# Performance work log

Hardware: AMD Instinct MI355X
Metric: run time of the kernel (lower is better)

Reference implementation:

```python
import jax, jax.numpy as jnp
from jax import lax
import numpy as np

B, L, NQ, NL, NC = 2048, 2048, 8, 3, 3  # batch, signal length, qubits, q-layers, classes


def setup_inputs() -> dict:
    key = jax.random.key(0)
    ks = jax.random.split(key, 20)
    rn = lambda k, shape, s=1.0: jax.random.normal(k, shape, jnp.float32) * s
    return dict(
        x_ecg=rn(ks[0], (B, 1, L)), x_eda=rn(ks[1], (B, 1, L)),
        x_emg=rn(ks[2], (B, 1, L)), x_resp=rn(ks[3], (B, 1, L)),
        conv1_w=rn(ks[4], (4, 16, 1, 3), 0.3), conv1_b=rn(ks[5], (4, 16), 0.05),
        conv2_w=rn(ks[6], (4, 32, 16, 3), 0.1), conv2_b=rn(ks[7], (4, 32), 0.05),
        lstm_w_ih=rn(ks[8], (4, 128, 32), 0.1), lstm_w_hh=rn(ks[9], (4, 128, 32), 0.1),
        lstm_b_ih=rn(ks[10], (4, 128), 0.05), lstm_b_hh=rn(ks[11], (4, 128), 0.05),
        bott_w=rn(ks[12], (8, 128), 0.08), bott_b=rn(ks[13], (8,), 0.05),
        q_weights=rn(ks[14], (NL, NQ, 3)),
        clf_w=rn(ks[15], (NC, 8), 0.3), clf_b=rn(ks[16], (NC,), 0.05),
    )


def _branch(x, c1w, c1b, c2w, c2b, wih, whh, bih, bhh):
    # x: [B,1,L]  ->  h_n: [B,32]
    dn = ('NCH', 'OIH', 'NCH')
    h = lax.conv_general_dilated(x, c1w, (1,), [(1, 1)], dimension_numbers=dn) + c1b[None, :, None]
    h = jax.nn.relu(h)
    h = h.reshape(h.shape[0], h.shape[1], -1, 2).max(-1)  # maxpool k=2
    h = lax.conv_general_dilated(h, c2w, (1,), [(1, 1)], dimension_numbers=dn) + c2b[None, :, None]
    h = jax.nn.relu(h)
    h = h.reshape(h.shape[0], h.shape[1], -1, 2).max(-1)  # [B,32,L//4]
    seq = jnp.swapaxes(h, 1, 2)  # [B,T,32]
    Bn, H = seq.shape[0], whh.shape[1]

    def step(carry, xt):
        hprev, cprev = carry
        gates = xt @ wih.T + hprev @ whh.T + bih + bhh  # [B,4H], torch gate order i,f,g,o
        i, f, g, o = jnp.split(gates, 4, axis=-1)
        c = jax.nn.sigmoid(f) * cprev + jax.nn.sigmoid(i) * jnp.tanh(g)
        hn = jax.nn.sigmoid(o) * jnp.tanh(c)
        return (hn, c), None

    init = (jnp.zeros((Bn, H), seq.dtype), jnp.zeros((Bn, H), seq.dtype))
    (h_n, _), _ = lax.scan(step, init, jnp.swapaxes(seq, 0, 1))
    return h_n


def _apply_1q(psi, gate, q, n):
    # psi: [B, 2^n]; gate: [2,2] (shared) or [B,2,2] (per-sample)
    Bn = psi.shape[0]
    left, right = 2 ** q, 2 ** (n - q - 1)
    s = psi.reshape(Bn, left, 2, right)
    if gate.ndim == 2:
        s = jnp.einsum('ij,bljr->blir', gate, s)
    else:
        s = jnp.einsum('bij,bljr->blir', gate, s)
    return s.reshape(Bn, -1)


def _apply_cnot(psi, c, t, n):
    # c < t always here
    Bn = psi.shape[0]
    s = psi.reshape(Bn, 2 ** c, 2, 2 ** (t - c - 1), 2, 2 ** (n - t - 1))
    s = s.at[:, :, 1].set(jnp.flip(s[:, :, 1], axis=3))
    return s.reshape(Bn, -1)


def _rz(a):
    e = jnp.exp(-0.5j * a)
    z = jnp.zeros_like(e)
    return jnp.stack([jnp.stack([e, z]), jnp.stack([z, jnp.conj(e)])])


def _ry(a):
    c, s = jnp.cos(a / 2), jnp.sin(a / 2)
    return jnp.stack([jnp.stack([c, -s]), jnp.stack([s, c])]).astype(jnp.complex64)


def _quantum(compressed, q_weights):
    # batched 8-qubit statevector simulation; compressed: [B, NQ]
    n = NQ
    Bn = compressed.shape[0]
    angles = compressed * jnp.pi
    psi = jnp.zeros((Bn, 2 ** n), jnp.complex64).at[:, 0].set(1.0)
    c, s = jnp.cos(angles / 2), jnp.sin(angles / 2)
    for q in range(n):  # RX embedding, per-sample gates
        g = jnp.stack([jnp.stack([c[:, q], -1j * s[:, q]], -1),
                       jnp.stack([-1j * s[:, q], c[:, q]], -1)], -2)  # [B,2,2]
        psi = _apply_1q(psi, g, q, n)
    for l in range(q_weights.shape[0]):
        for q in range(n):
            w = q_weights[l, q]
            # pennylane Rot(phi,theta,omega) = RZ(omega) @ RY(theta) @ RZ(phi)
            g = _rz(w[2]) @ _ry(w[1]) @ _rz(w[0])
            psi = _apply_1q(psi, g, q, n)
        stride = l + 1
        for q in range(n):
            t = q + stride
            if t < n:
                psi = _apply_cnot(psi, q, t, n)
    p = (jnp.abs(psi) ** 2).reshape((Bn,) + (2,) * n)
    zs = []
    for i in range(n):  # <Z_i> = P(|0>_i) - P(|1>_i)
        axes = tuple(a for a in range(1, n + 1) if a != i + 1)
        m = p.sum(axes)
        zs.append(m[:, 0] - m[:, 1])
    return jnp.stack(zs, -1).astype(jnp.float32)


def reference(x_ecg, x_eda, x_emg, x_resp, conv1_w, conv1_b, conv2_w, conv2_b,
              lstm_w_ih, lstm_w_hh, lstm_b_ih, lstm_b_hh, bott_w, bott_b,
              q_weights, clf_w, clf_b):
    xs = jnp.stack([x_ecg, x_eda, x_emg, x_resp])  # [4,B,1,L]
    feats = jax.vmap(_branch)(xs, conv1_w, conv1_b, conv2_w, conv2_b,
                              lstm_w_ih, lstm_w_hh, lstm_b_ih, lstm_b_hh)  # [4,B,32]
    combined = jnp.transpose(feats, (1, 0, 2)).reshape(feats.shape[1], -1)  # [B,128]
    compressed = jnp.tanh(combined @ bott_w.T + bott_b)  # [B,8]
    q_out = _quantum(compressed, q_weights)  # [B,8]
    logits = q_out @ clf_w.T + clf_b  # [B,3]
    return logits
```

## Files before the change

kernel.cpp:

```cpp
#include <hip/hip_runtime.h>
#include <hip/hip_bf16.h>

#define BATCH 2048
#define LSIG 2048
#define TSTEPS 512
#define CH 16
#define NCHUNK (TSTEPS / CH)

typedef float v2f __attribute__((ext_vector_type(2)));
typedef float v4f __attribute__((ext_vector_type(4)));
typedef __bf16 b16x8 __attribute__((ext_vector_type(8)));
typedef float f32x4 __attribute__((ext_vector_type(4)));
typedef unsigned int u32x4 __attribute__((ext_vector_type(4)));

#define PKFMA(d, a, b) asm("v_pk_fma_f32 %0, %1, %2, %0" : "+v"(d) : "v"(a), "v"(b))

__device__ __forceinline__ float sigf(float x) {
    return __fdividef(1.f, 1.f + __expf(-x));
}
__device__ __forceinline__ float tanhfast(float x) {
    return 1.f - __fdividef(2.f, __expf(2.f * x) + 1.f);
}
__device__ __forceinline__ unsigned short bf16rne(float f) {
    unsigned u = __float_as_uint(f);
    return (unsigned short)((u + 0x7FFFu + ((u >> 16) & 1u)) >> 16);
}
__device__ __forceinline__ unsigned cvtpk_bf16(float a, float b) {
    unsigned d;
    asm("v_cvt_pk_bf16_f32 %0, %1, %2" : "=v"(d) : "v"(a), "v"(b));
    return d;
}
__device__ __forceinline__ int swz(int co) {
    return (co < 16) ? ((co >> 2) * 8 + (co & 3))
                     : (((co >> 2) - 4) * 8 + 4 + (co & 3));
}

__global__ __launch_bounds__(64) void frontend_kernel(
    const float* __restrict__ x0, const float* __restrict__ x1,
    const float* __restrict__ x2, const float* __restrict__ x3,
    const float* __restrict__ c1w, const float* __restrict__ c1b,
    const float* __restrict__ c2w, const float* __restrict__ c2b,
    unsigned short* __restrict__ seqh, unsigned short* __restrict__ seql,
    int t0, int Tseg, int nck)
{
    const int s    = blockIdx.x;
    const int br   = blockIdx.y & 3;
    const int cko  = blockIdx.y >> 2;
    const int lane = threadIdx.x;
    const float* xg = (br == 0) ? x0 : (br == 1) ? x1 : (br == 2) ? x2 : x3;

    __shared__ float xs_c[70];
    __shared__ float p1buf[34][16];

    const int ci = lane & 15;
    const int co = lane & 31;
    const int hf = lane >> 5;
    const int sp = swz(co);

    const float w10 = c1w[br * 48 + ci * 3 + 0];
    const float w11 = c1w[br * 48 + ci * 3 + 1];
    const float w12 = c1w[br * 48 + ci * 3 + 2];
    const float b1v = c1b[br * 16 + ci];

    float wt[24];
    {
        const v4f* p = (const v4f*)(c2w + br * 1536 + co * 48 + hf * 24);
        #pragma unroll
        for (int i = 0; i < 6; ++i) ((v4f*)wt)[i] = p[i];
    }
    v4f w2p[3][2];
    #pragma unroll
    for (int k = 0; k < 3; ++k)
        #pragma unroll
        for (int h2 = 0; h2 < 2; ++h2)
            w2p[k][h2] = (v4f){ wt[(h2 * 4 + 0) * 3 + k], wt[(h2 * 4 + 1) * 3 + k],
                                wt[(h2 * 4 + 2) * 3 + k], wt[(h2 * 4 + 3) * 3 + k] };
    const float b2v = c2b[br * 32 + co];

    #pragma unroll 1
    for (int ic = 0; ic < nck; ++ic) {
        const int ck  = cko * nck + ic;
        const int tc0 = t0 + ck * CH;
        const int lt0 = ck * CH;

        __syncthreads();
        {
            int g = 4 * tc0 - 3 + lane;
            xs_c[lane] = ((unsigned)g < (unsigned)LSIG) ? xg[(size_t)s * LSIG + g] : 0.f;
            if (lane < 6) {
                int g2 = 4 * tc0 + 61 + lane;
                xs_c[64 + lane] = ((unsigned)g2 < (unsigned)LSIG) ? xg[(size_t)s * LSIG + g2] : 0.f;
            }
        }
        __syncthreads();

        #pragma unroll 1
        for (int it = 0; it < 9; ++it) {
            int idx = it * 64 + lane;
            if (idx < 34 * 16) {
                int pl = idx >> 4;
                float xa = xs_c[2 * pl + 0], xb = xs_c[2 * pl + 1];
                float xc = xs_c[2 * pl + 2], xd = xs_c[2 * pl + 3];
                float a0 = fmaf(xc, w12, fmaf(xb, w11, fmaf(xa, w10, b1v)));
                float a1 = fmaf(xd, w12, fmaf(xc, w11, fmaf(xb, w10, b1v)));
                float v = fmaxf(fmaxf(a0, a1), 0.f);
                int p1g = 2 * tc0 - 1 + pl;
                v = ((unsigned)p1g < (unsigned)(LSIG / 2)) ? v : 0.f;
                p1buf[pl][idx & 15] = v;
            }
        }
        __syncthreads();

        {
            const v4f* pbase = (const v4f*)&p1buf[0][0];
            const int h2o = hf * 2;
            v4f r0a = pbase[0 * 4 + h2o], r0b = pbase[0 * 4 + h2o + 1];
            v4f r1a = pbase[1 * 4 + h2o], r1b = pbase[1 * 4 + h2o + 1];
            v4f r2a = pbase[2 * 4 + h2o], r2b = pbase[2 * 4 + h2o + 1];
            v4f r3a = pbase[3 * 4 + h2o], r3b = pbase[3 * 4 + h2o + 1];
            #pragma unroll 1
            for (int tl = 0; tl < CH; ++tl) {
                v2f aA = {0.f, 0.f}, aB = {0.f, 0.f};
                PKFMA(aA, r0a.xy, w2p[0][0].xy); PKFMA(aA, r0a.zw, w2p[0][0].zw);
                PKFMA(aA, r0b.xy, w2p[0][1].xy); PKFMA(aA, r0b.zw, w2p[0][1].zw);
                PKFMA(aA, r1a.xy, w2p[1][0].xy); PKFMA(aA, r1a.zw, w2p[1][0].zw);
                PKFMA(aA, r1b.xy, w2p[1][1].xy); PKFMA(aA, r1b.zw, w2p[1][1].zw);
                PKFMA(aA, r2a.xy, w2p[2][0].xy); PKFMA(aA, r2a.zw, w2p[2][0].zw);
                PKFMA(aA, r2b.xy, w2p[2][1].xy); PKFMA(aA, r2b.zw, w2p[2][1].zw);
                PKFMA(aB, r1a.xy, w2p[0][0].xy); PKFMA(aB, r1a.zw, w2p[0][0].zw);
                PKFMA(aB, r1b.xy, w2p[0][1].xy); PKFMA(aB, r1b.zw, w2p[0][1].zw);
                PKFMA(aB, r2a.xy, w2p[1][0].xy); PKFMA(aB, r2a.zw, w2p[1][0].zw);
                PKFMA(aB, r2b.xy, w2p[1][1].xy); PKFMA(aB, r2b.zw, w2p[1][1].zw);
                PKFMA(aB, r3a.xy, w2p[2][0].xy); PKFMA(aB, r3a.zw, w2p[2][0].zw);
                PKFMA(aB, r3b.xy, w2p[2][1].xy); PKFMA(aB, r3b.zw, w2p[2][1].zw);
                float sA = aA.x + aA.y, sB = aB.x + aB.y;
                sA += __shfl_xor(sA, 32);
                sB += __shfl_xor(sB, 32);
                float sv = fmaxf(fmaxf(sA, sB) + b2v, 0.f);
                unsigned short hb = bf16rne(sv);
                float hif = __uint_as_float(((unsigned)hb) << 16);
                unsigned short lb = bf16rne(sv - hif);
                size_t off = (((size_t)br * Tseg + (lt0 + tl)) * 2048 + s) * 32 + sp;
                if (hf == 0) seqh[off] = hb;
                else         seql[off] = lb;
                r0a = r2a; r0b = r2b; r1a = r3a; r1b = r3b;
                if (tl < CH - 1) {
                    r2a = pbase[(2 * tl + 4) * 4 + h2o]; r2b = pbase[(2 * tl + 4) * 4 + h2o + 1];
                    r3a = pbase[(2 * tl + 5) * 4 + h2o]; r3b = pbase[(2 * tl + 5) * 4 + h2o + 1];
                }
            }
        }
    }
}

__global__ __launch_bounds__(64, 1) void lstm_mfma_kernel(
    const unsigned short* __restrict__ seqh, const unsigned short* __restrict__ seql,
    const float* __restrict__ wih, const float* __restrict__ whh,
    const float* __restrict__ bih, const float* __restrict__ bhh,
    float* __restrict__ state, float* __restrict__ feats,
    int t0, int Tseg)
{
    const int s0   = blockIdx.x * 16;
    const int br   = blockIdx.y;
    const int lane = threadIdx.x;
    const int c    = lane & 15;
    const int q    = lane >> 4;

    __shared__ f32x4 bias_lds[8][64];
    #pragma unroll
    for (int n = 0; n < 8; ++n) {
        f32x4 b;
        #pragma unroll
        for (int r = 0; r < 4; ++r) {
            int g = 16 * n + 4 * q + r;
            b[r] = bih[br * 128 + g] + bhh[br * 128 + g];
        }
        bias_lds[n][lane] = b;
    }
    __syncthreads();

    b16x8 wihhi[8], wihlo[8], whhhi[8], whhlo[8];
    #pragma unroll
    for (int n = 0; n < 8; ++n) {
        const int gr = 16 * n + c;
        const float* pi = wih + (size_t)br * 4096 + (size_t)gr * 32;
        const float* phw = whh + (size_t)br * 4096 + (size_t)gr * 32;
        v4f ia = *(const v4f*)(pi + 4 * q);
        v4f ib = *(const v4f*)(pi + 16 + 4 * q);
        v4f ha = *(const v4f*)(phw + 4 * q);
        v4f hb = *(const v4f*)(phw + 16 + 4 * q);
        #pragma unroll
        for (int j = 0; j < 4; ++j) {
            __bf16 t;
            t = (__bf16)ia[j]; wihhi[n][j]     = t; wihlo[n][j]     = (__bf16)(ia[j] - (float)t);
            t = (__bf16)ib[j]; wihhi[n][4 + j] = t; wihlo[n][4 + j] = (__bf16)(ib[j] - (float)t);
            t = (__bf16)ha[j]; whhhi[n][j]     = t; whhlo[n][j]     = (__bf16)(ha[j] - (float)t);
            t = (__bf16)hb[j]; whhhi[n][4 + j] = t; whhlo[n][4 + j] = (__bf16)(hb[j] - (float)t);
        }
    }

    b16x8 bhh_f, bhl_f;
    float cst[2][4];
    if (t0 == 0) {
        #pragma unroll
        for (int j = 0; j < 8; ++j) { bhh_f[j] = (__bf16)0.f; bhl_f[j] = (__bf16)0.f; }
        #pragma unroll
        for (int hh = 0; hh < 2; ++hh)
            #pragma unroll
            for (int r = 0; r < 4; ++r) cst[hh][r] = 0.f;
    } else {
        const float* st = state + (((size_t)br * BATCH + s0 + c) * 2) * 32;
        #pragma unroll
        for (int hh = 0; hh < 2; ++hh)
            #pragma unroll
            for (int r = 0; r < 4; ++r) {
                int u = 16 * hh + 4 * q + r;
                float hv = st[u];
                __bf16 hb2 = (__bf16)hv;
                bhh_f[hh * 4 + r] = hb2;
                bhl_f[hh * 4 + r] = (__bf16)(hv - (float)hb2);
                cst[hh][r] = st[32 + u];
            }
    }

    const size_t xbase = ((size_t)br * Tseg * 2048 + s0 + c) * 32 + (size_t)q * 8;
    const size_t xstep = 2048 * 32;
    const unsigned short* ph = seqh + xbase;
    const unsigned short* pl = seql + xbase;

    f32x4 xacc[8];
    b16x8 nh1, nl1;
    {
        b16x8 x0h = *(const b16x8*)ph;
        b16x8 x0l = *(const b16x8*)pl;
        #pragma unroll
        for (int n = 0; n < 8; ++n) {
            xacc[n] = __builtin_amdgcn_mfma_f32_16x16x32_bf16(wihhi[n], x0h, bias_lds[n][lane], 0, 0, 0);
            xacc[n] = __builtin_amdgcn_mfma_f32_16x16x32_bf16(wihhi[n], x0l, xacc[n], 0, 0, 0);
            xacc[n] = __builtin_amdgcn_mfma_f32_16x16x32_bf16(wihlo[n], x0h, xacc[n], 0, 0, 0);
        }
        nh1 = *(const b16x8*)(ph + xstep);
        nl1 = *(const b16x8*)(pl + xstep);
    }

#define STEP_BODY(LAST)                                                          \
    {                                                                            \
        _Pragma("unroll")                                                        \
        for (int n = 0; n < 8; ++n) {                                            \
            xacc[n] = __builtin_amdgcn_mfma_f32_16x16x32_bf16(whhhi[n], bhh_f, xacc[n], 0, 0, 0); \
            xacc[n] = __builtin_amdgcn_mfma_f32_16x16x32_bf16(whhhi[n], bhl_f, xacc[n], 0, 0, 0); \
            xacc[n] = __builtin_amdgcn_mfma_f32_16x16x32_bf16(whhlo[n], bhh_f, xacc[n], 0, 0, 0); \
        }                                                                        \
        float hv[8];                                                             \
        _Pragma("unroll")                                                        \
        for (int hh = 0; hh < 2; ++hh) {                                         \
            _Pragma("unroll")                                                    \
            for (int r = 0; r < 4; ++r) {                                        \
                float gi = xacc[0 + hh][r];                                      \
                float gf = xacc[2 + hh][r];                                      \
                float gg = xacc[4 + hh][r];                                      \
                float go = xacc[6 + hh][r];                                      \
                float si = sigf(gi);                                             \
                float sf = sigf(gf);                                             \
                float tg = tanhfast(gg);                                         \
                float so = sigf(go);                                             \
                float cc = fmaf(sf, cst[hh][r], si * tg);                        \
                cst[hh][r] = cc;                                                 \
                hv[hh * 4 + r] = so * tanhfast(cc);                              \
            }                                                                    \
        }                                                                        \
        u32x4 hd_, ld_;                                                          \
        _Pragma("unroll")                                                        \
        for (int p = 0; p < 4; ++p) {                                            \
            float a = hv[2 * p], b = hv[2 * p + 1];                              \
            unsigned d = cvtpk_bf16(a, b);                                       \
            float fa = __uint_as_float(d << 16);                                 \
            float fb = __uint_as_float(d & 0xFFFF0000u);                         \
            ld_[p] = cvtpk_bf16(a - fa, b - fb);                                 \
            hd_[p] = d;                                                          \
        }                                                                        \
        bhh_f = __builtin_bit_cast(b16x8, hd_);                                  \
        bhl_f = __builtin_bit_cast(b16x8, ld_);                                  \
        if (LAST) {                                                              \
            float* fp = feats + ((size_t)br * BATCH + s0 + c) * 32 + 4 * q;      \
            _Pragma("unroll")                                                    \
            for (int r = 0; r < 4; ++r) { fp[r] = hv[r]; fp[16 + r] = hv[4 + r]; } \
        }                                                                        \
    }

#define XACC_FROM(XH, XL)                                                        \
    {                                                                            \
        _Pragma("unroll")                                                        \
        for (int n = 0; n < 8; ++n) {                                            \
            xacc[n] = __builtin_amdgcn_mfma_f32_16x16x32_bf16(wihhi[n], XH, bias_lds[n][lane], 0, 0, 0); \
            xacc[n] = __builtin_amdgcn_mfma_f32_16x16x32_bf16(wihhi[n], XL, xacc[n], 0, 0, 0); \
            xacc[n] = __builtin_amdgcn_mfma_f32_16x16x32_bf16(wihlo[n], XH, xacc[n], 0, 0, 0); \
        }                                                                        \
    }

    #pragma unroll 1
    for (int t = 0; t < Tseg; t += 2) {
        b16x8 pbh, pbl;
        if (t + 2 < Tseg) {
            pbh = *(const b16x8*)(ph + (size_t)(t + 2) * xstep);
            pbl = *(const b16x8*)(pl + (size_t)(t + 2) * xstep);
        }
        STEP_BODY(false)
        XACC_FROM(nh1, nl1)

        const bool last = (t0 + t + 1 == TSTEPS - 1);
        if (t + 3 < Tseg) {
            nh1 = *(const b16x8*)(ph + (size_t)(t + 3) * xstep);
            nl1 = *(const b16x8*)(pl + (size_t)(t + 3) * xstep);
        }
        STEP_BODY(last)
        if (t + 2 < Tseg) { XACC_FROM(pbh, pbl) }
    }
#undef STEP_BODY
#undef XACC_FROM

    if (t0 + Tseg < TSTEPS) {
        float* st = state + (((size_t)br * BATCH + s0 + c) * 2) * 32;
        #pragma unroll
        for (int hh = 0; hh < 2; ++hh)
            #pragma unroll
            for (int r = 0; r < 4; ++r) {
                int u = 16 * hh + 4 * q + r;
                st[u]      = (float)bhh_f[hh * 4 + r] + (float)bhl_f[hh * 4 + r];
                st[32 + u] = cst[hh][r];
            }
    }
}

__global__ __launch_bounds__(64, 2) void branch_fallback(
    const float* __restrict__ x0, const float* __restrict__ x1,
    const float* __restrict__ x2, const float* __restrict__ x3,
    const float* __restrict__ c1w, const float* __restrict__ c1b,
    const float* __restrict__ c2w, const float* __restrict__ c2b,
    const float* __restrict__ wih, const float* __restrict__ whh,
    const float* __restrict__ bih, const float* __restrict__ bhh,
    float* __restrict__ feats)
{
    const int s    = blockIdx.x;
    const int br   = blockIdx.y;
    const int lane = threadIdx.x;
    const float* xg = (br == 0) ? x0 : (br == 1) ? x1 : (br == 2) ? x2 : x3;

    __shared__ float xs_c[70];
    __shared__ float p1buf[34][16];
    __shared__ float seqb[CH][32];
    __shared__ float hb[2][32];

    const int ci = lane & 15;
    const int co = lane & 31;
    const int hf = lane >> 5;

    const float bs0 = bih[br * 128 + lane]      + bhh[br * 128 + lane];
    const float bs1 = bih[br * 128 + lane + 64] + bhh[br * 128 + lane + 64];

    if (lane < 32) hb[0][lane] = 0.f;
    float c_state = 0.f;

    #pragma unroll 1
    for (int chk = 0; chk < NCHUNK; ++chk) {
        const int tc0 = chk * CH;
        {
            int g = 4 * tc0 - 3 + lane;
            xs_c[lane] = ((unsigned)g < (unsigned)LSIG) ? xg[(size_t)s * LSIG + g] : 0.f;
            if (lane < 6) {
                int g2 = 4 * tc0 + 61 + lane;
                xs_c[64 + lane] = ((unsigned)g2 < (unsigned)LSIG) ? xg[(size_t)s * LSIG + g2] : 0.f;
            }
        }
        const float* pc1 = c1w + br * 48 + ci * 3;  asm volatile("" : "+v"(pc1));
        const float w10 = pc1[0], w11 = pc1[1], w12 = pc1[2];
        const float* pb1 = c1b + br * 16 + ci;      asm volatile("" : "+v"(pb1));
        const float b1v = pb1[0];
        const float* pc2 = c2w + br * 1536 + co * 48 + hf * 24;
        asm volatile("" : "+v"(pc2));
        float wt[24];
        #pragma unroll
        for (int i = 0; i < 6; ++i) ((v4f*)wt)[i] = ((const v4f*)pc2)[i];
        v4f w2p[3][2];
        #pragma unroll
        for (int k = 0; k < 3; ++k)
            #pragma unroll
            for (int h2 = 0; h2 < 2; ++h2)
                w2p[k][h2] = (v4f){ wt[(h2 * 4 + 0) * 3 + k], wt[(h2 * 4 + 1) * 3 + k],
                                    wt[(h2 * 4 + 2) * 3 + k], wt[(h2 * 4 + 3) * 3 + k] };
        const float* pb2 = c2b + br * 32 + co;      asm volatile("" : "+v"(pb2));
        const float b2v = pb2[0];
        __syncthreads();
        #pragma unroll 1
        for (int it = 0; it < 9; ++it) {
            int idx = it * 64 + lane;
            if (idx < 34 * 16) {
                int pl = idx >> 4;
                float xa = xs_c[2 * pl + 0], xb = xs_c[2 * pl + 1];
                float xc = xs_c[2 * pl + 2], xd = xs_c[2 * pl + 3];
                float a0 = fmaf(xc, w12, fmaf(xb, w11, fmaf(xa, w10, b1v)));
                float a1 = fmaf(xd, w12, fmaf(xc, w11, fmaf(xb, w10, b1v)));
                float v = fmaxf(fmaxf(a0, a1), 0.f);
                int p1g = 2 * tc0 - 1 + pl;
                v = ((unsigned)p1g < (unsigned)(LSIG / 2)) ? v : 0.f;
                p1buf[pl][idx & 15] = v;
            }
        }
        __syncthreads();
        {
            const v4f* pbase = (const v4f*)&p1buf[0][0];
            const int h2o = hf * 2;
            v4f r0a = pbase[0 * 4 + h2o], r0b = pbase[0 * 4 + h2o + 1];
            v4f r1a = pbase[1 * 4 + h2o], r1b = pbase[1 * 4 + h2o + 1];
            v4f r2a = pbase[2 * 4 + h2o], r2b = pbase[2 * 4 + h2o + 1];
            v4f r3a = pbase[3 * 4 + h2o], r3b = pbase[3 * 4 + h2o + 1];
            #pragma unroll 1
            for (int tl = 0; tl < CH; ++tl) {
                v2f aA = {0.f, 0.f}, aB = {0.f, 0.f};
                PKFMA(aA, r0a.xy, w2p[0][0].xy); PKFMA(aA, r0a.zw, w2p[0][0].zw);
                PKFMA(aA, r0b.xy, w2p[0][1].xy); PKFMA(aA, r0b.zw, w2p[0][1].zw);
                PKFMA(aA, r1a.xy, w2p[1][0].xy); PKFMA(aA, r1a.zw, w2p[1][0].zw);
                PKFMA(aA, r1b.xy, w2p[1][1].xy); PKFMA(aA, r1b.zw, w2p[1][1].zw);
                PKFMA(aA, r2a.xy, w2p[2][0].xy); PKFMA(aA, r2a.zw, w2p[2][0].zw);
                PKFMA(aA, r2b.xy, w2p[2][1].xy); PKFMA(aA, r2b.zw, w2p[2][1].zw);
                PKFMA(aB, r1a.xy, w2p[0][0].xy); PKFMA(aB, r1a.zw, w2p[0][0].zw);
                PKFMA(aB, r1b.xy, w2p[0][1].xy); PKFMA(aB, r1b.zw, w2p[0][1].zw);
                PKFMA(aB, r2a.xy, w2p[1][0].xy); PKFMA(aB, r2a.zw, w2p[1][0].zw);
                PKFMA(aB, r2b.xy, w2p[1][1].xy); PKFMA(aB, r2b.zw, w2p[1][1].zw);
                PKFMA(aB, r3a.xy, w2p[2][0].xy); PKFMA(aB, r3a.zw, w2p[2][0].zw);
                PKFMA(aB, r3b.xy, w2p[2][1].xy); PKFMA(aB, r3b.zw, w2p[2][1].zw);
                float sA = aA.x + aA.y, sB = aB.x + aB.y;
                sA += __shfl_xor(sA, 32);
                sB += __shfl_xor(sB, 32);
                if (hf == 0)
                    seqb[tl][co] = fmaxf(fmaxf(sA, sB) + b2v, 0.f);
                r0a = r2a; r0b = r2b; r1a = r3a; r1b = r3b;
                if (tl < CH - 1) {
                    r2a = pbase[(2 * tl + 4) * 4 + h2o]; r2b = pbase[(2 * tl + 4) * 4 + h2o + 1];
                    r3a = pbase[(2 * tl + 5) * 4 + h2o]; r3b = pbase[(2 * tl + 5) * 4 + h2o + 1];
                }
            }
        }
        __syncthreads();
        float gpx0[CH], gpx1[CH];
        {
            const float* pwi = wih + (size_t)br * 4096 + (size_t)lane * 32;
            asm volatile("" : "+v"(pwi));
            v4f wiA[8], wiB[8];
            #pragma unroll
            for (int j = 0; j < 8; ++j) {
                wiA[j] = ((const v4f*)pwi)[j];
                wiB[j] = ((const v4f*)(pwi + 64 * 32))[j];
            }
            #pragma unroll
            for (int tl = 0; tl < CH; ++tl) {
                const v4f* xq = (const v4f*)&seqb[tl][0];
                v2f aA = {0.f, 0.f}, aB = {0.f, 0.f};
                #pragma unroll
                for (int j = 0; j < 8; ++j) {
                    v4f xv = xq[j];
                    PKFMA(aA, xv.xy, wiA[j].xy); PKFMA(aA, xv.zw, wiA[j].zw);
                    PKFMA(aB, xv.xy, wiB[j].xy); PKFMA(aB, xv.zw, wiB[j].zw);
                }
                gpx0[tl] = aA.x + aA.y;
                gpx1[tl] = aB.x + aB.y;
            }
        }
        {
            const float* pwh = whh + (size_t)br * 4096 + (size_t)lane * 32;
            asm volatile("" : "+v"(pwh));
            v4f whA[8], whB[8];
            #pragma unroll
            for (int j = 0; j < 8; ++j) {
                whA[j] = ((const v4f*)pwh)[j];
                whB[j] = ((const v4f*)(pwh + 64 * 32))[j];
            }
            #pragma unroll
            for (int tl = 0; tl < CH; ++tl) {
                __syncthreads();
                const int p = (tc0 + tl) & 1;
                const v4f* hq = (const v4f*)&hb[p][0];
                v2f aA = {0.f, 0.f}, aB = {0.f, 0.f};
                #pragma unroll
                for (int j = 0; j < 8; ++j) {
                    v4f hv = hq[j];
                    PKFMA(aA, hv.xy, whA[j].xy); PKFMA(aA, hv.zw, whA[j].zw);
                    PKFMA(aB, hv.xy, whB[j].xy); PKFMA(aB, hv.zw, whB[j].zw);
                }
                float g0 = bs0 + gpx0[tl] + aA.x + aA.y;
                float g1 = bs1 + gpx1[tl] + aB.x + aB.y;
                float a0 = sigf(g0);
                float earg = (lane < 32) ? 2.f * g1 : -g1;
                float e1 = __expf(fminf(earg, 80.f));
                float num = (lane < 32) ? e1 - 1.f : 1.f;
                float a1 = __fdividef(num, e1 + 1.f);
                float fa = __shfl_xor(a0, 32);
                float oa = __shfl_xor(a1, 32);
                if (lane < 32) {
                    c_state = fmaf(fa, c_state, a0 * a1);
                    hb[p ^ 1][lane] = oa * tanhfast(c_state);
                }
            }
        }
    }
    __syncthreads();
    if (lane < 32)
        feats[((size_t)br * BATCH + s) * 32 + lane] = hb[0][lane];
}


__device__ __forceinline__ void apply1q(float2* psi, int lane, int q,
                                        float2 g00, float2 g01,
                                        float2 g10, float2 g11)
{
    const int shift = 7 - q;
    const int right = 1 << shift;
    #pragma unroll
    for (int pp = 0; pp < 2; ++pp) {
        int p  = lane + 64 * pp;
        int l  = p >> shift;
        int r  = p & (right - 1);
        int i0 = (l << (shift + 1)) + r;
        int i1 = i0 + right;
        float2 a = psi[i0], b = psi[i1];
        float2 n0 = make_float2(g00.x * a.x - g00.y * a.y + g01.x * b.x - g01.y * b.y,
                                g00.x * a.y + g00.y * a.x + g01.x * b.y + g01.y * b.x);
        float2 n1 = make_float2(g10.x * a.x - g10.y * a.y + g11.x * b.x - g11.y * b.y,
                                g10.x * a.y + g10.y * a.x + g11.x * b.y + g11.y * b.x);
        psi[i0] = n0;
        psi[i1] = n1;
    }
    __syncthreads();
}

__global__ __launch_bounds__(64) void tail_kernel(
    const float* __restrict__ feats, const float* __restrict__ bw,
    const float* __restrict__ bb, const float* __restrict__ qw,
    const float* __restrict__ cw, const float* __restrict__ cb,
    float* __restrict__ out)
{
    const int s    = blockIdx.x;
    const int lane = threadIdx.x;

    __shared__ float comb[128];
    __shared__ float2 psi[256];
    __shared__ float ang[8];

    comb[lane]      = feats[(size_t)(lane >> 5) * (BATCH * 32) + (size_t)s * 32 + (lane & 31)];
    comb[lane + 64] = feats[(size_t)((lane + 64) >> 5) * (BATCH * 32) + (size_t)s * 32 + (lane & 31)];
    __syncthreads();

    {
        int q = lane >> 3, k0 = lane & 7;
        float p = 0.f;
        #pragma unroll
        for (int i = 0; i < 16; ++i) {
            int k = k0 + 8 * i;
            p = fmaf(comb[k], bw[q * 128 + k], p);
        }
        p += __shfl_xor(p, 4);
        p += __shfl_xor(p, 2);
        p += __shfl_xor(p, 1);
        if (k0 == 0) ang[q] = tanhf(p + bb[q]);
    }
    #pragma unroll
    for (int r = 0; r < 4; ++r) {
        int idx = lane + 64 * r;
        psi[idx] = make_float2(idx == 0 ? 1.f : 0.f, 0.f);
    }
    __syncthreads();

    const float PI_F = 3.14159265358979323846f;

    for (int q = 0; q < 8; ++q) {
        float half = ang[q] * PI_F * 0.5f;
        float cv = cosf(half), sv = sinf(half);
        apply1q(psi, lane, q,
                make_float2(cv, 0.f), make_float2(0.f, -sv),
                make_float2(0.f, -sv), make_float2(cv, 0.f));
    }

    for (int l = 0; l < 3; ++l) {
        for (int q = 0; q < 8; ++q) {
            float phi = qw[(l * 8 + q) * 3 + 0];
            float th  = qw[(l * 8 + q) * 3 + 1];
            float om  = qw[(l * 8 + q) * 3 + 2];
            float ct = cosf(0.5f * th), st = sinf(0.5f * th);
            float A = 0.5f * (phi + om), D = 0.5f * (phi - om);
            float cA = cosf(A), sA = sinf(A), cD = cosf(D), sD = sinf(D);
            apply1q(psi, lane, q,
                    make_float2(ct * cA, -ct * sA), make_float2(-st * cD, -st * sD),
                    make_float2(st * cD, -st * sD), make_float2(ct * cA,  ct * sA));
        }
        int stride = l + 1;
        for (int q = 0; q + stride < 8; ++q) {
            int cbit = 1 << (7 - q);
            int tbit = 1 << (7 - (q + stride));
            #pragma unroll
            for (int r = 0; r < 4; ++r) {
                int idx = lane + 64 * r;
                if ((idx & cbit) && !(idx & tbit)) {
                    int j = idx | tbit;
                    float2 tmp = psi[idx];
                    psi[idx] = psi[j];
                    psi[j] = tmp;
                }
            }
            __syncthreads();
        }
    }

    float z[8];
    #pragma unroll
    for (int q = 0; q < 8; ++q) z[q] = 0.f;
    #pragma unroll
    for (int r = 0; r < 4; ++r) {
        int idx = lane + 64 * r;
        float2 a = psi[idx];
        float pr = a.x * a.x + a.y * a.y;
        #pragma unroll
        for (int q = 0; q < 8; ++q)
            z[q] += (idx & (1 << (7 - q))) ? -pr : pr;
    }
    #pragma unroll
    for (int q = 0; q < 8; ++q) {
        #pragma unroll
        for (int off = 32; off; off >>= 1) z[q] += __shfl_xor(z[q], off);
    }
    if (lane == 0) {
        #pragma unroll
        for (int c = 0; c < 3; ++c) {
            float acc = cb[c];
            #pragma unroll
            for (int q = 0; q < 8; ++q) acc = fmaf(z[q], cw[c * 8 + q], acc);
            out[s * 3 + c] = acc;
        }
    }
}

extern "C" void kernel_launch(void* const* d_in, const int* in_sizes, int n_in,
                              void* d_out, int out_size, void* d_ws, size_t ws_size,
                              hipStream_t stream)
{
    (void)in_sizes; (void)n_in; (void)out_size;
    const float* x0  = (const float*)d_in[0];
    const float* x1  = (const float*)d_in[1];
    const float* x2  = (const float*)d_in[2];
    const float* x3  = (const float*)d_in[3];
    const float* c1w = (const float*)d_in[4];
    const float* c1b = (const float*)d_in[5];
    const float* c2w = (const float*)d_in[6];
    const float* c2b = (const float*)d_in[7];
    const float* wih = (const float*)d_in[8];
    const float* whh = (const float*)d_in[9];
    const float* bih = (const float*)d_in[10];
    const float* bhh = (const float*)d_in[11];
    const float* bw  = (const float*)d_in[12];
    const float* bb  = (const float*)d_in[13];
    const float* qw  = (const float*)d_in[14];
    const float* cw  = (const float*)d_in[15];
    const float* cb  = (const float*)d_in[16];

    const size_t state_b = 4ULL * BATCH * 64ULL * 4ULL;
    const size_t feats_b = 4ULL * BATCH * 32ULL * 4ULL;
    const size_t per_t   = 4ULL * 2048ULL * 32ULL * 4ULL;

    int Tseg = 0;
    for (int cand = 512; cand >= 32; cand >>= 1) {
        if ((size_t)cand * per_t + state_b + feats_b <= ws_size) { Tseg = cand; break; }
    }

    if (Tseg > 0) {
        size_t seg_elems = (size_t)Tseg * 4ULL * 2048ULL * 32ULL;
        unsigned short* seqh = (unsigned short*)d_ws;
        unsigned short* seql = seqh + seg_elems;
        float* state = (float*)((char*)d_ws + 2ULL * seg_elems * 2ULL);
        float* feats = (float*)((char*)state + state_b);

        const int slots = Tseg / CH;
        const int nck   = (slots >= 4) ? 4 : slots;

        for (int t0 = 0; t0 < TSTEPS; t0 += Tseg) {
            frontend_kernel<<<dim3(BATCH, 4 * (slots / nck)), 64, 0, stream>>>(
                x0, x1, x2, x3, c1w, c1b, c2w, c2b, seqh, seql, t0, Tseg, nck);
            lstm_mfma_kernel<<<dim3(BATCH / 16, 4), 64, 0, stream>>>(
                seqh, seql, wih, whh, bih, bhh, state, feats, t0, Tseg);
        }
        tail_kernel<<<BATCH, 64, 0, stream>>>(
            feats, bw, bb, qw, cw, cb, (float*)d_out);
    } else {
        float* feats = (float*)d_ws;
        branch_fallback<<<dim3(BATCH, 4), 64, 0, stream>>>(
            x0, x1, x2, x3, c1w, c1b, c2w, c2b, wih, whh, bih, bhh, feats);
        tail_kernel<<<BATCH, 64, 0, stream>>>(
            feats, bw, bb, qw, cw, cb, (float*)d_out);
    }
}
```

Baseline: 1.438 ms.

## Fuse frontend and LSTM into one launch, pipelining segments with double buffering

```diff
diff --git a/kernel.cpp b/kernel.cpp
--- a/kernel.cpp
+++ b/kernel.cpp
@@ -7,6 +7,12 @@
 #define CH 16
 #define NCHUNK (TSTEPS / CH)
 
+#define TSEG 64
+#define SLOTS (TSEG / CH)
+#define NCK 4
+#define FE_BLOCKS (BATCH * 4 * (SLOTS / NCK))
+#define LSTM_BLOCKS ((BATCH / 16) * 4)
+
 typedef float v2f __attribute__((ext_vector_type(2)));
 typedef float v4f __attribute__((ext_vector_type(4)));
 typedef __bf16 b16x8 __attribute__((ext_vector_type(8)));
@@ -35,23 +41,14 @@
                      : (((co >> 2) - 4) * 8 + 4 + (co & 3));
 }
 
-__global__ __launch_bounds__(64) void frontend_kernel(
-    const float* __restrict__ x0, const float* __restrict__ x1,
-    const float* __restrict__ x2, const float* __restrict__ x3,
-    const float* __restrict__ c1w, const float* __restrict__ c1b,
-    const float* __restrict__ c2w, const float* __restrict__ c2b,
-    unsigned short* __restrict__ seqh, unsigned short* __restrict__ seql,
-    int t0, int Tseg, int nck)
-{
-    const int s    = blockIdx.x;
-    const int br   = blockIdx.y & 3;
-    const int cko  = blockIdx.y >> 2;
-    const int lane = threadIdx.x;
-    const float* xg = (br == 0) ? x0 : (br == 1) ? x1 : (br == 2) ? x2 : x3;
-
-    __shared__ float xs_c[70];
-    __shared__ float p1buf[34][16];
-
+__device__ void fe_body(
+    int s, int br, int cko, int lane,
+    const float* xg, const float* c1w, const float* c1b,
+    const float* c2w, const float* c2b,
+    unsigned short* seqh, unsigned short* seql,
+    int t0, int Tseg, int nck,
+    float* xs_c, float (*p1buf)[16])
+{
     const int ci = lane & 15;
     const int co = lane & 31;
     const int hf = lane >> 5;
@@ -153,20 +150,17 @@
     }
 }
 
-__global__ __launch_bounds__(64, 1) void lstm_mfma_kernel(
-    const unsigned short* __restrict__ seqh, const unsigned short* __restrict__ seql,
-    const float* __restrict__ wih, const float* __restrict__ whh,
-    const float* __restrict__ bih, const float* __restrict__ bhh,
-    float* __restrict__ state, float* __restrict__ feats,
-    int t0, int Tseg)
-{
-    const int s0   = blockIdx.x * 16;
-    const int br   = blockIdx.y;
-    const int lane = threadIdx.x;
-    const int c    = lane & 15;
-    const int q    = lane >> 4;
-
-    __shared__ f32x4 bias_lds[8][64];
+__device__ void lstm_body(
+    int s0, int br, int lane,
+    const unsigned short* seqh, const unsigned short* seql,
+    const float* wih, const float* whh,
+    const float* bih, const float* bhh,
+    float* state, float* feats,
+    int t0, int Tseg, f32x4 (*bias_lds)[64])
+{
+    const int c = lane & 15;
+    const int q = lane >> 4;
+
     #pragma unroll
     for (int n = 0; n < 8; ++n) {
         f32x4 b;
@@ -332,180 +326,70 @@
     }
 }
 
-__global__ __launch_bounds__(64, 2) void branch_fallback(
+__global__ __launch_bounds__(64, 1) void fused_kernel(
     const float* __restrict__ x0, const float* __restrict__ x1,
     const float* __restrict__ x2, const float* __restrict__ x3,
     const float* __restrict__ c1w, const float* __restrict__ c1b,
     const float* __restrict__ c2w, const float* __restrict__ c2b,
+    const unsigned short* __restrict__ seqAh, const unsigned short* __restrict__ seqAl,
+    unsigned short* __restrict__ seqBh, unsigned short* __restrict__ seqBl,
     const float* __restrict__ wih, const float* __restrict__ whh,
     const float* __restrict__ bih, const float* __restrict__ bhh,
-    float* __restrict__ feats)
-{
-    const int s    = blockIdx.x;
-    const int br   = blockIdx.y;
-    const int lane = threadIdx.x;
-    const float* xg = (br == 0) ? x0 : (br == 1) ? x1 : (br == 2) ? x2 : x3;
-
+    float* __restrict__ state, float* __restrict__ feats,
+    int t0_lstm, int t0_fe)
+{
+    __shared__ f32x4 bias_lds[8][64];
     __shared__ float xs_c[70];
     __shared__ float p1buf[34][16];
-    __shared__ float seqb[CH][32];
-    __shared__ float hb[2][32];
-
-    const int ci = lane & 15;
-    const int co = lane & 31;
-    const int hf = lane >> 5;
-
-    const float bs0 = bih[br * 128 + lane]      + bhh[br * 128 + lane];
-    const float bs1 = bih[br * 128 + lane + 64] + bhh[br * 128 + lane + 64];
-
-    if (lane < 32) hb[0][lane] = 0.f;
-    float c_state = 0.f;
-
-    #pragma unroll 1
-    for (int chk = 0; chk < NCHUNK; ++chk) {
-        const int tc0 = chk * CH;
-        {
-            int g = 4 * tc0 - 3 + lane;
-            xs_c[lane] = ((unsigned)g < (unsigned)LSIG) ? xg[(size_t)s * LSIG + g] : 0.f;
-            if (lane < 6) {
-                int g2 = 4 * tc0 + 61 + lane;
-                xs_c[64 + lane] = ((unsigned)g2 < (unsigned)LSIG) ? xg[(size_t)s * LSIG + g2] : 0.f;
-            }
-        }
-        const float* pc1 = c1w + br * 48 + ci * 3;  asm volatile("" : "+v"(pc1));
-        const float w10 = pc1[0], w11 = pc1[1], w12 = pc1[2];
-        const float* pb1 = c1b + br * 16 + ci;      asm volatile("" : "+v"(pb1));
-        const float b1v = pb1[0];
-        const float* pc2 = c2w + br * 1536 + co * 48 + hf * 24;
-        asm volatile("" : "+v"(pc2));
-        float wt[24];
-        #pragma unroll
-        for (int i = 0; i < 6; ++i) ((v4f*)wt)[i] = ((const v4f*)pc2)[i];
-        v4f w2p[3][2];
-        #pragma unroll
-        for (int k = 0; k < 3; ++k)
-            #pragma unroll
-            for (int h2 = 0; h2 < 2; ++h2)
-                w2p[k][h2] = (v4f){ wt[(h2 * 4 + 0) * 3 + k], wt[(h2 * 4 + 1) * 3 + k],
-                                    wt[(h2 * 4 + 2) * 3 + k], wt[(h2 * 4 + 3) * 3 + k] };
-        const float* pb2 = c2b + br * 32 + co;      asm volatile("" : "+v"(pb2));
-        const float b2v = pb2[0];
-        __syncthreads();
-        #pragma unroll 1
-        for (int it = 0; it < 9; ++it) {
-            int idx = it * 64 + lane;
-            if (idx < 34 * 16) {
-                int pl = idx >> 4;
-                float xa = xs_c[2 * pl + 0], xb = xs_c[2 * pl + 1];
-                float xc = xs_c[2 * pl + 2], xd = xs_c[2 * pl + 3];
-                float a0 = fmaf(xc, w12, fmaf(xb, w11, fmaf(xa, w10, b1v)));
-                float a1 = fmaf(xd, w12, fmaf(xc, w11, fmaf(xb, w10, b1v)));
-                float v = fmaxf(fmaxf(a0, a1), 0.f);
-                int p1g = 2 * tc0 - 1 + pl;
-                v = ((unsigned)p1g < (unsigned)(LSIG / 2)) ? v : 0.f;
-                p1buf[pl][idx & 15] = v;
-            }
-        }
-        __syncthreads();
-        {
-            const v4f* pbase = (const v4f*)&p1buf[0][0];
-            const int h2o = hf * 2;
-            v4f r0a = pbase[0 * 4 + h2o], r0b = pbase[0 * 4 + h2o + 1];
-            v4f r1a = pbase[1 * 4 + h2o], r1b = pbase[1 * 4 + h2o + 1];
-            v4f r2a = pbase[2 * 4 + h2o], r2b = pbase[2 * 4 + h2o + 1];
-            v4f r3a = pbase[3 * 4 + h2o], r3b = pbase[3 * 4 + h2o + 1];
-            #pragma unroll 1
-            for (int tl = 0; tl < CH; ++tl) {
-                v2f aA = {0.f, 0.f}, aB = {0.f, 0.f};
-                PKFMA(aA, r0a.xy, w2p[0][0].xy); PKFMA(aA, r0a.zw, w2p[0][0].zw);
-                PKFMA(aA, r0b.xy, w2p[0][1].xy); PKFMA(aA, r0b.zw, w2p[0][1].zw);
-                PKFMA(aA, r1a.xy, w2p[1][0].xy); PKFMA(aA, r1a.zw, w2p[1][0].zw);
-                PKFMA(aA, r1b.xy, w2p[1][1].xy); PKFMA(aA, r1b.zw, w2p[1][1].zw);
-                PKFMA(aA, r2a.xy, w2p[2][0].xy); PKFMA(aA, r2a.zw, w2p[2][0].zw);
-                PKFMA(aA, r2b.xy, w2p[2][1].xy); PKFMA(aA, r2b.zw, w2p[2][1].zw);
-                PKFMA(aB, r1a.xy, w2p[0][0].xy); PKFMA(aB, r1a.zw, w2p[0][0].zw);
-                PKFMA(aB, r1b.xy, w2p[0][1].xy); PKFMA(aB, r1b.zw, w2p[0][1].zw);
-                PKFMA(aB, r2a.xy, w2p[1][0].xy); PKFMA(aB, r2a.zw, w2p[1][0].zw);
-                PKFMA(aB, r2b.xy, w2p[1][1].xy); PKFMA(aB, r2b.zw, w2p[1][1].zw);
-                PKFMA(aB, r3a.xy, w2p[2][0].xy); PKFMA(aB, r3a.zw, w2p[2][0].zw);
-                PKFMA(aB, r3b.xy, w2p[2][1].xy); PKFMA(aB, r3b.zw, w2p[2][1].zw);
-                float sA = aA.x + aA.y, sB = aB.x + aB.y;
-                sA += __shfl_xor(sA, 32);
-                sB += __shfl_xor(sB, 32);
-                if (hf == 0)
-                    seqb[tl][co] = fmaxf(fmaxf(sA, sB) + b2v, 0.f);
-                r0a = r2a; r0b = r2b; r1a = r3a; r1b = r3b;
-                if (tl < CH - 1) {
-                    r2a = pbase[(2 * tl + 4) * 4 + h2o]; r2b = pbase[(2 * tl + 4) * 4 + h2o + 1];
-                    r3a = pbase[(2 * tl + 5) * 4 + h2o]; r3b = pbase[(2 * tl + 5) * 4 + h2o + 1];
-                }
-            }
-        }
-        __syncthreads();
-        float gpx0[CH], gpx1[CH];
-        {
-            const float* pwi = wih + (size_t)br * 4096 + (size_t)lane * 32;
-            asm volatile("" : "+v"(pwi));
-            v4f wiA[8], wiB[8];
-            #pragma unroll
-            for (int j = 0; j < 8; ++j) {
-                wiA[j] = ((const v4f*)pwi)[j];
-                wiB[j] = ((const v4f*)(pwi + 64 * 32))[j];
-            }
-            #pragma unroll
-            for (int tl = 0; tl < CH; ++tl) {
-                const v4f* xq = (const v4f*)&seqb[tl][0];
-                v2f aA = {0.f, 0.f}, aB = {0.f, 0.f};
-                #pragma unroll
-                for (int j = 0; j < 8; ++j) {
-                    v4f xv = xq[j];
-                    PKFMA(aA, xv.xy, wiA[j].xy); PKFMA(aA, xv.zw, wiA[j].zw);
-                    PKFMA(aB, xv.xy, wiB[j].xy); PKFMA(aB, xv.zw, wiB[j].zw);
-                }
-                gpx0[tl] = aA.x + aA.y;
-                gpx1[tl] = aB.x + aB.y;
-            }
-        }
-        {
-            const float* pwh = whh + (size_t)br * 4096 + (size_t)lane * 32;
-            asm volatile("" : "+v"(pwh));
-            v4f whA[8], whB[8];
-            #pragma unroll
-            for (int j = 0; j < 8; ++j) {
-                whA[j] = ((const v4f*)pwh)[j];
-                whB[j] = ((const v4f*)(pwh + 64 * 32))[j];
-            }
-            #pragma unroll
-            for (int tl = 0; tl < CH; ++tl) {
-                __syncthreads();
-                const int p = (tc0 + tl) & 1;
-                const v4f* hq = (const v4f*)&hb[p][0];
-                v2f aA = {0.f, 0.f}, aB = {0.f, 0.f};
-                #pragma unroll
-                for (int j = 0; j < 8; ++j) {
-                    v4f hv = hq[j];
-                    PKFMA(aA, hv.xy, whA[j].xy); PKFMA(aA, hv.zw, whA[j].zw);
-                    PKFMA(aB, hv.xy, whB[j].xy); PKFMA(aB, hv.zw, whB[j].zw);
-                }
-                float g0 = bs0 + gpx0[tl] + aA.x + aA.y;
-                float g1 = bs1 + gpx1[tl] + aB.x + aB.y;
-                float a0 = sigf(g0);
-                float earg = (lane < 32) ? 2.f * g1 : -g1;
-                float e1 = __expf(fminf(earg, 80.f));
-                float num = (lane < 32) ? e1 - 1.f : 1.f;
-                float a1 = __fdividef(num, e1 + 1.f);
-                float fa = __shfl_xor(a0, 32);
-                float oa = __shfl_xor(a1, 32);
-                if (lane < 32) {
-                    c_state = fmaf(fa, c_state, a0 * a1);
-                    hb[p ^ 1][lane] = oa * tanhfast(c_state);
-                }
-            }
-        }
-    }
-    __syncthreads();
-    if (lane < 32)
-        feats[((size_t)br * BATCH + s) * 32 + lane] = hb[0][lane];
+
+    const int bx   = blockIdx.x;
+    const int lane = threadIdx.x;
+
+    if (bx < LSTM_BLOCKS) {
+        const int br = bx / (BATCH / 16);
+        const int s0 = (bx % (BATCH / 16)) * 16;
+        lstm_body(s0, br, lane, seqAh, seqAl, wih, whh, bih, bhh,
+                  state, feats, t0_lstm, TSEG, bias_lds);
+    } else {
+        const int fid = bx - LSTM_BLOCKS;
+        const int s   = fid & (BATCH - 1);
+        const int yy  = fid >> 11;
+        const int br  = yy & 3;
+        const int cko = yy >> 2;
+        const float* xg = (br == 0) ? x0 : (br == 1) ? x1 : (br == 2) ? x2 : x3;
+        fe_body(s, br, cko, lane, xg, c1w, c1b, c2w, c2b,
+                seqBh, seqBl, t0_fe, TSEG, NCK, xs_c, p1buf);
+    }
+}
+
+__global__ __launch_bounds__(64) void frontend_kernel(
+    const float* __restrict__ x0, const float* __restrict__ x1,
+    const float* __restrict__ x2, const float* __restrict__ x3,
+    const float* __restrict__ c1w, const float* __restrict__ c1b,
+    const float* __restrict__ c2w, const float* __restrict__ c2b,
+    unsigned short* __restrict__ seqh, unsigned short* __restrict__ seql,
+    int t0, int Tseg, int nck)
+{
+    __shared__ float xs_c[70];
+    __shared__ float p1buf[34][16];
+    const int s   = blockIdx.x;
+    const int br  = blockIdx.y & 3;
+    const int cko = blockIdx.y >> 2;
+    const float* xg = (br == 0) ? x0 : (br == 1) ? x1 : (br == 2) ? x2 : x3;
+    fe_body(s, br, cko, threadIdx.x, xg, c1w, c1b, c2w, c2b,
+            seqh, seql, t0, Tseg, nck, xs_c, p1buf);
+}
+
+__global__ __launch_bounds__(64, 1) void lstm_mfma_kernel(
+    const unsigned short* __restrict__ seqh, const unsigned short* __restrict__ seql,
+    const float* __restrict__ wih, const float* __restrict__ whh,
+    const float* __restrict__ bih, const float* __restrict__ bhh,
+    float* __restrict__ state, float* __restrict__ feats,
+    int t0, int Tseg)
+{
+    __shared__ f32x4 bias_lds[8][64];
+    lstm_body(blockIdx.x * 16, blockIdx.y, threadIdx.x, seqh, seql,
+              wih, whh, bih, bhh, state, feats, t0, Tseg, bias_lds);
 }
 
 
@@ -664,22 +548,45 @@
     const size_t state_b = 4ULL * BATCH * 64ULL * 4ULL;
     const size_t feats_b = 4ULL * BATCH * 32ULL * 4ULL;
     const size_t per_t   = 4ULL * 2048ULL * 32ULL * 4ULL;
-
-    int Tseg = 0;
-    for (int cand = 512; cand >= 32; cand >>= 1) {
-        if ((size_t)cand * per_t + state_b + feats_b <= ws_size) { Tseg = cand; break; }
-    }
-
-    if (Tseg > 0) {
-        size_t seg_elems = (size_t)Tseg * 4ULL * 2048ULL * 32ULL;
+    const size_t seg_e   = (size_t)TSEG * 4ULL * 2048ULL * 32ULL;
+
+    if (2ULL * (size_t)TSEG * per_t + state_b + feats_b <= ws_size) {
+        unsigned short* bufh[2];
+        unsigned short* bufl[2];
+        bufh[0] = (unsigned short*)d_ws;
+        bufl[0] = bufh[0] + seg_e;
+        bufh[1] = bufl[0] + seg_e;
+        bufl[1] = bufh[1] + seg_e;
+        float* state = (float*)((char*)d_ws + 4ULL * seg_e * 2ULL);
+        float* feats = (float*)((char*)state + state_b);
+
+        const int nseg = TSTEPS / TSEG;
+        frontend_kernel<<<dim3(BATCH, 4 * (SLOTS / NCK)), 64, 0, stream>>>(
+            x0, x1, x2, x3, c1w, c1b, c2w, c2b, bufh[0], bufl[0], 0, TSEG, NCK);
+        for (int i = 0; i < nseg; ++i) {
+            const int cur = i & 1, nxt = cur ^ 1;
+            const bool has_fe = (i + 1 < nseg);
+            const int nblk = LSTM_BLOCKS + (has_fe ? FE_BLOCKS : 0);
+            fused_kernel<<<nblk, 64, 0, stream>>>(
+                x0, x1, x2, x3, c1w, c1b, c2w, c2b,
+                bufh[cur], bufl[cur], bufh[nxt], bufl[nxt],
+                wih, whh, bih, bhh, state, feats,
+                i * TSEG, (i + 1) * TSEG);
+        }
+        tail_kernel<<<BATCH, 64, 0, stream>>>(
+            feats, bw, bb, qw, cw, cb, (float*)d_out);
+    } else {
+        int Tseg = 0;
+        for (int cand = 512; cand >= 16; cand >>= 1) {
+            if ((size_t)cand * per_t + state_b + feats_b <= ws_size) { Tseg = cand; break; }
+        }
+        size_t se = (size_t)Tseg * 4ULL * 2048ULL * 32ULL;
         unsigned short* seqh = (unsigned short*)d_ws;
-        unsigned short* seql = seqh + seg_elems;
-        float* state = (float*)((char*)d_ws + 2ULL * seg_elems * 2ULL);
+        unsigned short* seql = seqh + se;
+        float* state = (float*)((char*)d_ws + 2ULL * se * 2ULL);
         float* feats = (float*)((char*)state + state_b);
-
         const int slots = Tseg / CH;
         const int nck   = (slots >= 4) ? 4 : slots;
-
         for (int t0 = 0; t0 < TSTEPS; t0 += Tseg) {
             frontend_kernel<<<dim3(BATCH, 4 * (slots / nck)), 64, 0, stream>>>(
                 x0, x1, x2, x3, c1w, c1b, c2w, c2b, seqh, seql, t0, Tseg, nck);
@@ -688,11 +595,5 @@
         }
         tail_kernel<<<BATCH, 64, 0, stream>>>(
             feats, bw, bb, qw, cw, cb, (float*)d_out);
-    } else {
-        float* feats = (float*)d_ws;
-        branch_fallback<<<dim3(BATCH, 4), 64, 0, stream>>>(
-            x0, x1, x2, x3, c1w, c1b, c2w, c2b, wih, whh, bih, bhh, feats);
-        tail_kernel<<<BATCH, 64, 0, stream>>>(
-            feats, bw, bb, qw, cw, cb, (float*)d_out);
-    }
-}
+    }
+}
```

New measurement: 1.944 ms. +35.2%, slower.
